# Performance work log

Hardware: AMD Instinct MI355X
Metric: run time of the kernel (lower is better)

The kernel has to match this reference:

```python
import jax, jax.numpy as jnp
import numpy as np

B, S, E = 64, 512, 1024   # batch, seq_len, enc_size (bert-large hidden)
P, K, C = 200, 10, 3      # num_prototypes, proto_size, num_classes


def setup_inputs() -> dict:
    key = jax.random.key(0)
    k1, k2, k3 = jax.random.split(key, 3)
    embedding = jax.random.normal(k1, (B, S, E), dtype=jnp.float32)
    # protolayer initialized with nn.init.uniform_ -> U[0,1)
    protolayer = jax.random.uniform(k2, (P, K, E), dtype=jnp.float32)
    fc_weight = jax.random.normal(k3, (C, P), dtype=jnp.float32) * 0.05
    return {"embedding": embedding, "protolayer": protolayer, "fc_weight": fc_weight}


def reference(embedding, protolayer, fc_weight):
    # torch.cdist(embedding[:,None], protolayer, p=2) broadcasts to [B,P,S,K]:
    # distances[b,p,s,k] = ||embedding[b,s,:] - protolayer[p,k,:]||_2
    x2 = jnp.sum(embedding * embedding, axis=-1)            # [B,S]
    y2 = jnp.sum(protolayer * protolayer, axis=-1)          # [P,K]
    xy = jnp.einsum('bse,pke->bpsk', embedding, protolayer) # [B,P,S,K]
    d2 = x2[:, None, :, None] + y2[None, :, None, :] - 2.0 * xy
    distances = jnp.sqrt(jnp.maximum(d2, 0.0))              # [B,P,S,K]
    # -max_pool2d(-d, kernel=(S,1)) == min over seq dim
    min_distances = jnp.min(distances, axis=2)               # [B,P,K]
    prototype_distances = jnp.mean(min_distances, axis=-1)   # [B,P]
    class_out = prototype_distances @ fc_weight.T            # [B,C]
    return prototype_distances, distances, class_out
```

## Files before the change

kernel.cpp:

```cpp
#include <hip/hip_runtime.h>
#include <hip/hip_bf16.h>

#define B_ 64
#define S_ 512
#define E_ 1024
#define P_ 200
#define K_ 10
#define C_ 3

#define BM 256
#define BN 80
#define BKS 64
#define NSTAGE (E_ / BKS)
#define NROWS_A (B_ * S_)
#define NROWS_B (P_ * K_)
#define NROWS_T (NROWS_A + NROWS_B)
#define NMT 128
#define NNT 25

typedef __attribute__((ext_vector_type(8))) short short8;
typedef __attribute__((ext_vector_type(4))) float f32x4;

__device__ __forceinline__ float bf2f(unsigned short u) {
    unsigned int x = ((unsigned int)u) << 16;
    return __uint_as_float(x);
}
__device__ __forceinline__ unsigned short f2bf(float f) {
    __hip_bfloat16 h = __float2bfloat16(f);
    unsigned short u;
    __builtin_memcpy(&u, &h, 2);
    return u;
}

__device__ __forceinline__ int swz(int row, int kbyte) {
    return (row * (BKS * 2) + kbyte) ^ ((row & 7) << 4);
}

#define GLDS16(gsrc, ldst)                                                              \
    __builtin_amdgcn_global_load_lds((const __attribute__((address_space(1))) unsigned int*)(gsrc), \
                                     (__attribute__((address_space(3))) unsigned int*)(ldst), 16, 0, 0)

__global__ __launch_bounds__(256) void preconvert(const float* __restrict__ emb,
                                                  const float* __restrict__ proto,
                                                  unsigned short* __restrict__ bf,
                                                  float* __restrict__ xy2) {
    const int row  = blockIdx.x * 4 + (threadIdx.x >> 6);
    const int lane = threadIdx.x & 63;
    const float* src = (row < NROWS_A) ? emb + (size_t)row * E_
                                       : proto + (size_t)(row - NROWS_A) * E_;
    unsigned short* dst = bf + (size_t)row * E_;
    float s = 0.f;
#pragma unroll
    for (int p = 0; p < 4; ++p) {
        float4 v = *(const float4*)(src + p * 256 + lane * 4);
        ushort4 h = { f2bf(v.x), f2bf(v.y), f2bf(v.z), f2bf(v.w) };
        float a = bf2f(h.x), b = bf2f(h.y), c = bf2f(h.z), d = bf2f(h.w);
        s += a * a + b * b + c * c + d * d;
        *(ushort4*)(dst + p * 256 + lane * 4) = h;
    }
#pragma unroll
    for (int off = 32; off > 0; off >>= 1) s += __shfl_xor(s, off);
    if (lane == 0) xy2[row] = s;
}

__global__ __launch_bounds__(512) void dist_gemm_bf(const unsigned short* __restrict__ Abf,
                                                    const unsigned short* __restrict__ Bbf,
                                                    const float* __restrict__ x2g,
                                                    const float* __restrict__ y2g,
                                                    float* __restrict__ dist,
                                                    float* __restrict__ ws_min) {
    __shared__ __align__(16) unsigned char smem[86016];
    __shared__ float red[8][BN];

    unsigned short* AsBase = (unsigned short*)smem;
    unsigned short* BsBase = (unsigned short*)(smem + 2 * BM * BKS * 2);
    float* Ch = (float*)smem;

    const int tid  = threadIdx.x;
    const int lane = tid & 63;
    const int wv   = tid >> 6;
    const int l15  = lane & 15;
    const int lh   = lane >> 4;

    const int id = blockIdx.x;
    const int sw = (id & 7) * (3200 / 8) + (id >> 3);
    const int nt = sw % NNT;
    const int mt = sw / NNT;

    const unsigned short* aSrc[4];
    unsigned lOffA[4];
#pragma unroll
    for (int i = 0; i < 4; ++i) {
        int idx = i * 512 + wv * 64 + lane;
        int r = idx >> 3, c = idx & 7;
        aSrc[i]  = Abf + (size_t)(mt * BM + r) * E_ + (c ^ (r & 7)) * 8;
        lOffA[i] = (unsigned)(i * 512 + wv * 64) * 8;
    }
    const unsigned short* bSrc[2];
    unsigned lOffB[2];
    {
        int idx = wv * 64 + lane;
        int r = idx >> 3, c = idx & 7;
        bSrc[0]  = Bbf + (size_t)(nt * BN + r) * E_ + (c ^ (r & 7)) * 8;
        lOffB[0] = (unsigned)(wv * 64) * 8;
    }
    {
        int idx = 512 + wv * 64 + lane;
        int r = idx >> 3, c = idx & 7;
        bSrc[1]  = Bbf + (size_t)(nt * BN + (r < BN ? r : 0)) * E_ + (c ^ (r & 7)) * 8;
        lOffB[1] = (unsigned)(512 + wv * 64) * 8;
    }

    f32x4 acc[2][5];
#pragma unroll
    for (int i = 0; i < 2; ++i)
#pragma unroll
        for (int j = 0; j < 5; ++j) acc[i][j] = (f32x4){0.f, 0.f, 0.f, 0.f};

#define ISSUE(tt, bb)                                                          \
    do {                                                                       \
        const size_t ko_ = (size_t)(tt) * BKS;                                 \
        unsigned short* Asb_ = AsBase + (bb) * (BM * BKS);                     \
        unsigned short* Bsb_ = BsBase + (bb) * (BN * BKS);                     \
        _Pragma("unroll")                                                      \
        for (int i_ = 0; i_ < 4; ++i_) GLDS16(aSrc[i_] + ko_, Asb_ + lOffA[i_]); \
        GLDS16(bSrc[0] + ko_, Bsb_ + lOffB[0]);                                \
        if (wv < 2) GLDS16(bSrc[1] + ko_, Bsb_ + lOffB[1]);                    \
    } while (0)

#define COMPUTE(bb)                                                            \
    do {                                                                       \
        const char* Ab_ = (const char*)(AsBase + (bb) * (BM * BKS));           \
        const char* Bb_ = (const char*)(BsBase + (bb) * (BN * BKS));           \
        _Pragma("unroll")                                                      \
        for (int kk = 0; kk < 2; ++kk) {                                       \
            const int kbyte = kk * 64 + lh * 16;                               \
            short8 af[2];                                                      \
            _Pragma("unroll")                                                  \
            for (int mf = 0; mf < 2; ++mf)                                     \
                af[mf] = *(const short8*)(Ab_ + swz(wv * 32 + mf * 16 + l15, kbyte)); \
            short8 bfr[5];                                                     \
            _Pragma("unroll")                                                  \
            for (int nf = 0; nf < 5; ++nf)                                     \
                bfr[nf] = *(const short8*)(Bb_ + swz(nf * 16 + l15, kbyte));   \
            _Pragma("unroll")                                                  \
            for (int mf = 0; mf < 2; ++mf)                                     \
                _Pragma("unroll")                                              \
                for (int nf = 0; nf < 5; ++nf)                                 \
                    acc[mf][nf] = __builtin_amdgcn_mfma_f32_16x16x32_bf16(     \
                        af[mf], bfr[nf], acc[mf][nf], 0, 0, 0);                \
        }                                                                      \
    } while (0)

    ISSUE(0, 0);
    __syncthreads();

    int buf = 0;
    for (int t = 0; t < NSTAGE; ++t) {
        if (t + 1 < NSTAGE) ISSUE(t + 1, buf ^ 1);
        COMPUTE(buf);
        __syncthreads();
        buf ^= 1;
    }
#undef ISSUE
#undef COMPUTE

    const int b  = mt >> 1;
    const int s0 = (mt & 1) * 256;

    float y2v[5];
#pragma unroll
    for (int nf = 0; nf < 5; ++nf) y2v[nf] = y2g[nt * BN + nf * 16 + l15];

    float mloc[5];
#pragma unroll
    for (int nf = 0; nf < 5; ++nf) mloc[nf] = 3.4e38f;

#define CH(blk, row, col) Ch[(((blk) * 16) + (row)) * 82 + (col)]

#pragma unroll
    for (int h = 0; h < 2; ++h) {
#pragma unroll
        for (int rg = 0; rg < 4; ++rg) {
            float x2 = x2g[mt * BM + wv * 32 + h * 16 + lh * 4 + rg];
#pragma unroll
            for (int nf = 0; nf < 5; ++nf) {
                float d2 = x2 + y2v[nf] - 2.f * acc[h][nf][rg];
                float d  = sqrtf(fmaxf(d2, 0.f));
                mloc[nf] = fminf(mloc[nf], d);
                CH(wv, lh * 4 + rg, nf * 16 + l15) = d;
            }
        }
        __syncthreads();

#pragma unroll
        for (int i = 0; i < 5; ++i) {
            int fid = i * 512 + tid;
            int r   = fid / 40;
            int q   = fid - r * 40;
            int p8  = r >> 3;
            int blk = r & 7;
            int e   = 4 * q;
            f32x4 v;
            v.x = CH(blk, (e + 0) / 10, p8 * 10 + (e + 0) % 10);
            v.y = CH(blk, (e + 1) / 10, p8 * 10 + (e + 1) % 10);
            v.z = CH(blk, (e + 2) / 10, p8 * 10 + (e + 2) % 10);
            v.w = CH(blk, (e + 3) / 10, p8 * 10 + (e + 3) % 10);
            int s_start = s0 + blk * 32 + h * 16;
            size_t base = ((size_t)(b * P_ + nt * 8 + p8) * S_ + s_start) * 10 + e;
            __builtin_nontemporal_store(v, (f32x4*)(dist + base));
        }
        __syncthreads();
    }
#undef CH

#pragma unroll
    for (int nf = 0; nf < 5; ++nf) {
        mloc[nf] = fminf(mloc[nf], __shfl_xor(mloc[nf], 16));
        mloc[nf] = fminf(mloc[nf], __shfl_xor(mloc[nf], 32));
    }
    if (lane < 16) {
#pragma unroll
        for (int nf = 0; nf < 5; ++nf) red[wv][nf * 16 + lane] = mloc[nf];
    }
    __syncthreads();
    if (tid < BN) {
        float v = red[0][tid];
#pragma unroll
        for (int w = 1; w < 8; ++w) v = fminf(v, red[w][tid]);
        ws_min[(size_t)mt * NROWS_B + nt * BN + tid] = v;
    }
}

__global__ __launch_bounds__(256) void mean_fc(const float* __restrict__ ws_min,
                                               const float* __restrict__ fcw,
                                               float* __restrict__ pd,
                                               float* __restrict__ cls) {
    const int b = blockIdx.x;
    const int t = threadIdx.x;
    __shared__ float pds[P_];
    if (t < P_) {
        float sum = 0.f;
#pragma unroll
        for (int k = 0; k < K_; ++k) {
            float m = fminf(ws_min[(size_t)(b * 2 + 0) * NROWS_B + t * K_ + k],
                            ws_min[(size_t)(b * 2 + 1) * NROWS_B + t * K_ + k]);
            sum += m;
        }
        float v = sum * (1.0f / K_);
        pd[b * P_ + t] = v;
        pds[t] = v;
    }
    __syncthreads();
    if (t < C_) {
        float s = 0.f;
        for (int p = 0; p < P_; ++p) s += pds[p] * fcw[t * P_ + p];
        cls[b * C_ + t] = s;
    }
}

#define FBM 128
#define FBN 80
#define FBKS 64
#define FNST 16
__device__ __forceinline__ int swzf(int row, int kbyte) {
    return (row * (FBKS * 2) + kbyte) ^ ((row & 7) << 4);
}
__global__ __launch_bounds__(256) void dist_mfma_fb(const float* __restrict__ emb,
                                                    const float* __restrict__ proto,
                                                    float* __restrict__ dist) {
    __shared__ short As[FBM * FBKS];
    __shared__ short Bs[FBN * FBKS];
    __shared__ float x2s[FBM];
    __shared__ float y2s[FBN];

    const int tid  = threadIdx.x;
    const int lane = tid & 63;
    const int wv   = tid >> 6;
    const int l15  = lane & 15;
    const int lh   = lane >> 4;

    const int id = blockIdx.x;
    const int sw = (id & 7) * (6400 / 8) + (id >> 3);
    const int nt = sw % 25;
    const int mt = sw / 25;

    const float* Ab = emb + (size_t)mt * FBM * E_ + (size_t)(tid >> 4) * E_ + (tid & 15) * 4;
    const float* Bb = proto + (size_t)nt * FBN * E_ + (size_t)(tid >> 4) * E_ + (tid & 15) * 4;

    f32x4 acc[2][5];
#pragma unroll
    for (int i = 0; i < 2; ++i)
#pragma unroll
        for (int j = 0; j < 5; ++j) acc[i][j] = (f32x4){0.f, 0.f, 0.f, 0.f};

    float x2p[8], y2p[5];
#pragma unroll
    for (int i = 0; i < 8; ++i) x2p[i] = 0.f;
#pragma unroll
    for (int i = 0; i < 5; ++i) y2p[i] = 0.f;

    float4 pa[8], pb[5];
#pragma unroll
    for (int i = 0; i < 8; ++i) pa[i] = *(const float4*)(Ab + (size_t)i * 16 * E_);
#pragma unroll
    for (int i = 0; i < 5; ++i) pb[i] = *(const float4*)(Bb + (size_t)i * 16 * E_);

    for (int t = 0; t < FNST; ++t) {
        ushort4 ca[8];
#pragma unroll
        for (int i = 0; i < 8; ++i) {
            float4 v = pa[i];
            x2p[i] += v.x * v.x + v.y * v.y + v.z * v.z + v.w * v.w;
            ca[i] = (ushort4){ f2bf(v.x), f2bf(v.y), f2bf(v.z), f2bf(v.w) };
        }
        ushort4 cb[5];
#pragma unroll
        for (int i = 0; i < 5; ++i) {
            float4 v = pb[i];
            y2p[i] += v.x * v.x + v.y * v.y + v.z * v.z + v.w * v.w;
            cb[i] = (ushort4){ f2bf(v.x), f2bf(v.y), f2bf(v.z), f2bf(v.w) };
        }
        __syncthreads();
#pragma unroll
        for (int i = 0; i < 8; ++i) {
            int idx = i * 256 + tid;
            *(ushort4*)((char*)As + swzf(idx >> 4, (idx & 15) * 8)) = ca[i];
        }
#pragma unroll
        for (int i = 0; i < 5; ++i) {
            int idx = i * 256 + tid;
            *(ushort4*)((char*)Bs + swzf(idx >> 4, (idx & 15) * 8)) = cb[i];
        }
        __syncthreads();
        if (t + 1 < FNST) {
            const float* An = Ab + (size_t)(t + 1) * FBKS;
            const float* Bn = Bb + (size_t)(t + 1) * FBKS;
#pragma unroll
            for (int i = 0; i < 8; ++i) pa[i] = *(const float4*)(An + (size_t)i * 16 * E_);
#pragma unroll
            for (int i = 0; i < 5; ++i) pb[i] = *(const float4*)(Bn + (size_t)i * 16 * E_);
        }
#pragma unroll
        for (int kk = 0; kk < 2; ++kk) {
            const int kbyte = kk * 64 + lh * 16;
            short8 af[2];
#pragma unroll
            for (int mf = 0; mf < 2; ++mf)
                af[mf] = *(const short8*)((const char*)As + swzf(wv * 32 + mf * 16 + l15, kbyte));
            short8 bfr[5];
#pragma unroll
            for (int nf = 0; nf < 5; ++nf)
                bfr[nf] = *(const short8*)((const char*)Bs + swzf(nf * 16 + l15, kbyte));
#pragma unroll
            for (int mf = 0; mf < 2; ++mf)
#pragma unroll
                for (int nf = 0; nf < 5; ++nf)
                    acc[mf][nf] = __builtin_amdgcn_mfma_f32_16x16x32_bf16(
                        af[mf], bfr[nf], acc[mf][nf], 0, 0, 0);
        }
    }

#pragma unroll
    for (int i = 0; i < 8; ++i) {
        float v = x2p[i];
        v += __shfl_xor(v, 1); v += __shfl_xor(v, 2);
        v += __shfl_xor(v, 4); v += __shfl_xor(v, 8);
        if (l15 == 0) x2s[16 * i + (tid >> 4)] = v;
    }
#pragma unroll
    for (int i = 0; i < 5; ++i) {
        float v = y2p[i];
        v += __shfl_xor(v, 1); v += __shfl_xor(v, 2);
        v += __shfl_xor(v, 4); v += __shfl_xor(v, 8);
        if (l15 == 0) y2s[16 * i + (tid >> 4)] = v;
    }
    __syncthreads();

#pragma unroll
    for (int mf = 0; mf < 2; ++mf) {
#pragma unroll
        for (int nf = 0; nf < 5; ++nf) {
#pragma unroll
            for (int rg = 0; rg < 4; ++rg) {
                int ml = wv * 32 + mf * 16 + lh * 4 + rg;
                int nl = nf * 16 + l15;
                int m = mt * FBM + ml;
                int n = nt * FBN + nl;
                int b = m >> 9;
                int s = m & (S_ - 1);
                int p = n / K_;
                int k = n - p * K_;
                float d2 = x2s[ml] + y2s[nl] - 2.f * acc[mf][nf][rg];
                dist[(((size_t)b * P_ + p) * S_ + s) * K_ + k] = sqrtf(fmaxf(d2, 0.f));
            }
        }
    }
}

__global__ __launch_bounds__(256) void min_mean(const float* __restrict__ dist,
                                                float* __restrict__ pd) {
    const int p = blockIdx.x;
    const int b = blockIdx.y;
    const float* dp = dist + ((size_t)b * P_ + p) * (size_t)(S_ * K_);
    const int tid = threadIdx.x;

    const float4* base = (const float4*)(dp + (size_t)tid * 20);
    float4 q0 = base[0], q1 = base[1], q2 = base[2], q3 = base[3], q4 = base[4];

    float mn[K_];
    mn[0] = fminf(q0.x, q2.z); mn[1] = fminf(q0.y, q2.w);
    mn[2] = fminf(q0.z, q3.x); mn[3] = fminf(q0.w, q3.y);
    mn[4] = fminf(q1.x, q3.z); mn[5] = fminf(q1.y, q3.w);
    mn[6] = fminf(q1.z, q4.x); mn[7] = fminf(q1.w, q4.y);
    mn[8] = fminf(q2.x, q4.z); mn[9] = fminf(q2.y, q4.w);

#pragma unroll
    for (int k = 0; k < K_; ++k) {
#pragma unroll
        for (int off = 32; off > 0; off >>= 1)
            mn[k] = fminf(mn[k], __shfl_xor(mn[k], off));
    }

    __shared__ float red[4][K_];
    if ((tid & 63) == 0) {
#pragma unroll
        for (int k = 0; k < K_; ++k) red[tid >> 6][k] = mn[k];
    }
    __syncthreads();
    if (tid == 0) {
        float sum = 0.f;
#pragma unroll
        for (int k = 0; k < K_; ++k)
            sum += fminf(fminf(red[0][k], red[1][k]), fminf(red[2][k], red[3][k]));
        pd[b * P_ + p] = sum * (1.0f / K_);
    }
}

__global__ void fc_kernel(const float* __restrict__ pd, const float* __restrict__ fc,
                          float* __restrict__ cls) {
    int tid = threadIdx.x;
    if (tid < B_ * C_) {
        int b = tid / C_;
        int c = tid % C_;
        float s = 0.f;
        for (int p = 0; p < P_; ++p) s += pd[b * P_ + p] * fc[c * P_ + p];
        cls[b * C_ + c] = s;
    }
}

extern "C" void kernel_launch(void* const* d_in, const int* in_sizes, int n_in,
                              void* d_out, int out_size, void* d_ws, size_t ws_size,
                              hipStream_t stream) {
    const float* emb   = (const float*)d_in[0];
    const float* proto = (const float*)d_in[1];
    const float* fc    = (const float*)d_in[2];
    float* out = (float*)d_out;

    float* pd   = out;
    float* dist = out + (size_t)B_ * P_;
    float* cls  = out + (size_t)B_ * P_ + (size_t)B_ * P_ * S_ * K_;

    const size_t bf_bytes  = (size_t)NROWS_T * E_ * 2;
    const size_t xy2_bytes = (size_t)NROWS_T * 4;
    const size_t min_bytes = (size_t)NMT * NROWS_B * 4;
    const size_t ws_need   = bf_bytes + xy2_bytes + min_bytes;

    if (ws_size >= ws_need) {
        unsigned short* bf = (unsigned short*)d_ws;
        float* xy2    = (float*)((char*)d_ws + bf_bytes);
        float* ws_min = (float*)((char*)d_ws + bf_bytes + xy2_bytes);
        preconvert<<<NROWS_T / 4, 256, 0, stream>>>(emb, proto, bf, xy2);
        dist_gemm_bf<<<NMT * NNT, 512, 0, stream>>>(bf, bf + (size_t)NROWS_A * E_,
                                                    xy2, xy2 + NROWS_A, dist, ws_min);
        mean_fc<<<B_, 256, 0, stream>>>(ws_min, fc, pd, cls);
    } else {
        dist_mfma_fb<<<6400, 256, 0, stream>>>(emb, proto, dist);
        min_mean<<<dim3(P_, B_), 256, 0, stream>>>(dist, pd);
        fc_kernel<<<1, 256, 0, stream>>>(pd, fc, cls);
    }
}
```

Baseline: 292.6 us.

## Double GEMM N-tile to 160 with 4x2 wave layout and zero-padded prototypes

Widens the distance GEMM tile from 80 to 160 prototype rows. Waves are rearranged into a 4x2 grid, each computing a 64x80 sub-tile, so every A tile loaded into LDS is reused across twice as many columns and A-side global and LDS traffic is halved. Prototype rows are zero-padded up to 13*160 in the preconvert kernel, and the epilogue skips stores for padded prototypes. In exchange the kernel needs more LDS and accumulator registers, launches fewer blocks, and spends some work on padding.

```diff
diff --git a/kernel.cpp b/kernel.cpp
--- a/kernel.cpp
+++ b/kernel.cpp
@@ -9,14 +9,15 @@
 #define C_ 3
 
 #define BM 256
-#define BN 80
+#define BN 160
 #define BKS 64
 #define NSTAGE (E_ / BKS)
 #define NROWS_A (B_ * S_)
 #define NROWS_B (P_ * K_)
-#define NROWS_T (NROWS_A + NROWS_B)
 #define NMT 128
-#define NNT 25
+#define NNT 13
+#define NBPAD (NNT * BN)
+#define NROWS_P (NROWS_A + NBPAD)
 
 typedef __attribute__((ext_vector_type(8))) short short8;
 typedef __attribute__((ext_vector_type(4))) float f32x4;
@@ -46,9 +47,17 @@
                                                   float* __restrict__ xy2) {
     const int row  = blockIdx.x * 4 + (threadIdx.x >> 6);
     const int lane = threadIdx.x & 63;
+    unsigned short* dst = bf + (size_t)row * E_;
+
+    if (row >= NROWS_A + NROWS_B) {
+        ushort4 z = {0, 0, 0, 0};
+#pragma unroll
+        for (int p = 0; p < 4; ++p) *(ushort4*)(dst + p * 256 + lane * 4) = z;
+        if (lane == 0) xy2[row] = 0.f;
+        return;
+    }
     const float* src = (row < NROWS_A) ? emb + (size_t)row * E_
                                        : proto + (size_t)(row - NROWS_A) * E_;
-    unsigned short* dst = bf + (size_t)row * E_;
     float s = 0.f;
 #pragma unroll
     for (int p = 0; p < 4; ++p) {
@@ -69,8 +78,8 @@
                                                     const float* __restrict__ y2g,
                                                     float* __restrict__ dist,
                                                     float* __restrict__ ws_min) {
-    __shared__ __align__(16) unsigned char smem[86016];
-    __shared__ float red[8][BN];
+    __shared__ __align__(16) unsigned char smem[106496];
+    __shared__ float red[8][80];
 
     unsigned short* AsBase = (unsigned short*)smem;
     unsigned short* BsBase = (unsigned short*)(smem + 2 * BM * BKS * 2);
@@ -79,11 +88,13 @@
     const int tid  = threadIdx.x;
     const int lane = tid & 63;
     const int wv   = tid >> 6;
+    const int wm   = wv >> 1;
+    const int wn   = wv & 1;
     const int l15  = lane & 15;
     const int lh   = lane >> 4;
 
     const int id = blockIdx.x;
-    const int sw = (id & 7) * (3200 / 8) + (id >> 3);
+    const int sw = (id & 7) * (1664 / 8) + (id >> 3);
     const int nt = sw % NNT;
     const int mt = sw / NNT;
 
@@ -91,29 +102,30 @@
     unsigned lOffA[4];
 #pragma unroll
     for (int i = 0; i < 4; ++i) {
-        int idx = i * 512 + wv * 64 + lane;
+        int idx = i * 512 + tid;
         int r = idx >> 3, c = idx & 7;
         aSrc[i]  = Abf + (size_t)(mt * BM + r) * E_ + (c ^ (r & 7)) * 8;
         lOffA[i] = (unsigned)(i * 512 + wv * 64) * 8;
     }
-    const unsigned short* bSrc[2];
-    unsigned lOffB[2];
+    const unsigned short* bSrc[3];
+    unsigned lOffB[3];
+#pragma unroll
+    for (int i = 0; i < 2; ++i) {
+        int idx = i * 512 + tid;
+        int r = idx >> 3, c = idx & 7;
+        bSrc[i]  = Bbf + (size_t)(nt * BN + r) * E_ + (c ^ (r & 7)) * 8;
+        lOffB[i] = (unsigned)(i * 512 + wv * 64) * 8;
+    }
     {
-        int idx = wv * 64 + lane;
+        int idx = 1024 + wv * 64 + lane;
         int r = idx >> 3, c = idx & 7;
-        bSrc[0]  = Bbf + (size_t)(nt * BN + r) * E_ + (c ^ (r & 7)) * 8;
-        lOffB[0] = (unsigned)(wv * 64) * 8;
-    }
-    {
-        int idx = 512 + wv * 64 + lane;
-        int r = idx >> 3, c = idx & 7;
-        bSrc[1]  = Bbf + (size_t)(nt * BN + (r < BN ? r : 0)) * E_ + (c ^ (r & 7)) * 8;
-        lOffB[1] = (unsigned)(512 + wv * 64) * 8;
-    }
-
-    f32x4 acc[2][5];
-#pragma unroll
-    for (int i = 0; i < 2; ++i)
+        bSrc[2]  = Bbf + (size_t)(nt * BN + (r < BN ? r : 0)) * E_ + (c ^ (r & 7)) * 8;
+        lOffB[2] = (unsigned)(1024 + wv * 64) * 8;
+    }
+
+    f32x4 acc[4][5];
+#pragma unroll
+    for (int i = 0; i < 4; ++i)
 #pragma unroll
         for (int j = 0; j < 5; ++j) acc[i][j] = (f32x4){0.f, 0.f, 0.f, 0.f};
 
@@ -124,8 +136,9 @@
         unsigned short* Bsb_ = BsBase + (bb) * (BN * BKS);                     \
         _Pragma("unroll")                                                      \
         for (int i_ = 0; i_ < 4; ++i_) GLDS16(aSrc[i_] + ko_, Asb_ + lOffA[i_]); \
-        GLDS16(bSrc[0] + ko_, Bsb_ + lOffB[0]);                                \
-        if (wv < 2) GLDS16(bSrc[1] + ko_, Bsb_ + lOffB[1]);                    \
+        _Pragma("unroll")                                                      \
+        for (int i_ = 0; i_ < 2; ++i_) GLDS16(bSrc[i_] + ko_, Bsb_ + lOffB[i_]); \
+        if (wv < 4) GLDS16(bSrc[2] + ko_, Bsb_ + lOffB[2]);                    \
     } while (0)
 
 #define COMPUTE(bb)                                                            \
@@ -135,16 +148,16 @@
         _Pragma("unroll")                                                      \
         for (int kk = 0; kk < 2; ++kk) {                                       \
             const int kbyte = kk * 64 + lh * 16;                               \
-            short8 af[2];                                                      \
+            short8 af[4];                                                      \
             _Pragma("unroll")                                                  \
-            for (int mf = 0; mf < 2; ++mf)                                     \
-                af[mf] = *(const short8*)(Ab_ + swz(wv * 32 + mf * 16 + l15, kbyte)); \
+            for (int mf = 0; mf < 4; ++mf)                                     \
+                af[mf] = *(const short8*)(Ab_ + swz(wm * 64 + mf * 16 + l15, kbyte)); \
             short8 bfr[5];                                                     \
             _Pragma("unroll")                                                  \
             for (int nf = 0; nf < 5; ++nf)                                     \
-                bfr[nf] = *(const short8*)(Bb_ + swz(nf * 16 + l15, kbyte));   \
+                bfr[nf] = *(const short8*)(Bb_ + swz(wn * 80 + nf * 16 + l15, kbyte)); \
             _Pragma("unroll")                                                  \
-            for (int mf = 0; mf < 2; ++mf)                                     \
+            for (int mf = 0; mf < 4; ++mf)                                     \
                 _Pragma("unroll")                                              \
                 for (int nf = 0; nf < 5; ++nf)                                 \
                     acc[mf][nf] = __builtin_amdgcn_mfma_f32_16x16x32_bf16(     \
@@ -170,25 +183,25 @@
 
     float y2v[5];
 #pragma unroll
-    for (int nf = 0; nf < 5; ++nf) y2v[nf] = y2g[nt * BN + nf * 16 + l15];
+    for (int nf = 0; nf < 5; ++nf) y2v[nf] = y2g[nt * BN + wn * 80 + nf * 16 + l15];
 
     float mloc[5];
 #pragma unroll
     for (int nf = 0; nf < 5; ++nf) mloc[nf] = 3.4e38f;
 
-#define CH(blk, row, col) Ch[(((blk) * 16) + (row)) * 82 + (col)]
-
-#pragma unroll
-    for (int h = 0; h < 2; ++h) {
+#define CH(slab, row, col) Ch[(((slab) * 16) + (row)) * 162 + (col)]
+
+#pragma unroll
+    for (int mf = 0; mf < 4; ++mf) {
 #pragma unroll
         for (int rg = 0; rg < 4; ++rg) {
-            float x2 = x2g[mt * BM + wv * 32 + h * 16 + lh * 4 + rg];
+            float x2 = x2g[mt * BM + wm * 64 + mf * 16 + lh * 4 + rg];
 #pragma unroll
             for (int nf = 0; nf < 5; ++nf) {
-                float d2 = x2 + y2v[nf] - 2.f * acc[h][nf][rg];
+                float d2 = x2 + y2v[nf] - 2.f * acc[mf][nf][rg];
                 float d  = sqrtf(fmaxf(d2, 0.f));
                 mloc[nf] = fminf(mloc[nf], d);
-                CH(wv, lh * 4 + rg, nf * 16 + l15) = d;
+                CH(wm, lh * 4 + rg, wn * 80 + nf * 16 + l15) = d;
             }
         }
         __syncthreads();
@@ -198,17 +211,20 @@
             int fid = i * 512 + tid;
             int r   = fid / 40;
             int q   = fid - r * 40;
-            int p8  = r >> 3;
-            int blk = r & 7;
+            int p16 = r >> 2;
+            int slab= r & 3;
             int e   = 4 * q;
-            f32x4 v;
-            v.x = CH(blk, (e + 0) / 10, p8 * 10 + (e + 0) % 10);
-            v.y = CH(blk, (e + 1) / 10, p8 * 10 + (e + 1) % 10);
-            v.z = CH(blk, (e + 2) / 10, p8 * 10 + (e + 2) % 10);
-            v.w = CH(blk, (e + 3) / 10, p8 * 10 + (e + 3) % 10);
-            int s_start = s0 + blk * 32 + h * 16;
-            size_t base = ((size_t)(b * P_ + nt * 8 + p8) * S_ + s_start) * 10 + e;
-            __builtin_nontemporal_store(v, (f32x4*)(dist + base));
+            int p   = nt * 16 + p16;
+            if (p < P_) {
+                f32x4 v;
+                v.x = CH(slab, (e + 0) / 10, p16 * 10 + (e + 0) % 10);
+                v.y = CH(slab, (e + 1) / 10, p16 * 10 + (e + 1) % 10);
+                v.z = CH(slab, (e + 2) / 10, p16 * 10 + (e + 2) % 10);
+                v.w = CH(slab, (e + 3) / 10, p16 * 10 + (e + 3) % 10);
+                int s_start = s0 + slab * 64 + mf * 16;
+                size_t base = ((size_t)(b * P_ + p) * S_ + s_start) * 10 + e;
+                __builtin_nontemporal_store(v, (f32x4*)(dist + base));
+            }
         }
         __syncthreads();
     }
@@ -225,10 +241,11 @@
     }
     __syncthreads();
     if (tid < BN) {
-        float v = red[0][tid];
-#pragma unroll
-        for (int w = 1; w < 8; ++w) v = fminf(v, red[w][tid]);
-        ws_min[(size_t)mt * NROWS_B + nt * BN + tid] = v;
+        int wn_ = tid / 80;
+        int cl  = tid - wn_ * 80;
+        float v = fminf(fminf(red[0 * 2 + wn_][cl], red[1 * 2 + wn_][cl]),
+                        fminf(red[2 * 2 + wn_][cl], red[3 * 2 + wn_][cl]));
+        ws_min[(size_t)mt * NBPAD + nt * BN + tid] = v;
     }
 }
 
@@ -243,8 +260,8 @@
         float sum = 0.f;
 #pragma unroll
         for (int k = 0; k < K_; ++k) {
-            float m = fminf(ws_min[(size_t)(b * 2 + 0) * NROWS_B + t * K_ + k],
-                            ws_min[(size_t)(b * 2 + 1) * NROWS_B + t * K_ + k]);
+            float m = fminf(ws_min[(size_t)(b * 2 + 0) * NBPAD + t * K_ + k],
+                            ws_min[(size_t)(b * 2 + 1) * NBPAD + t * K_ + k]);
             sum += m;
         }
         float v = sum * (1.0f / K_);
@@ -461,16 +478,16 @@
     float* dist = out + (size_t)B_ * P_;
     float* cls  = out + (size_t)B_ * P_ + (size_t)B_ * P_ * S_ * K_;
 
-    const size_t bf_bytes  = (size_t)NROWS_T * E_ * 2;
-    const size_t xy2_bytes = (size_t)NROWS_T * 4;
-    const size_t min_bytes = (size_t)NMT * NROWS_B * 4;
+    const size_t bf_bytes  = (size_t)NROWS_P * E_ * 2;
+    const size_t xy2_bytes = (size_t)NROWS_P * 4;
+    const size_t min_bytes = (size_t)NMT * NBPAD * 4;
     const size_t ws_need   = bf_bytes + xy2_bytes + min_bytes;
 
     if (ws_size >= ws_need) {
         unsigned short* bf = (unsigned short*)d_ws;
         float* xy2    = (float*)((char*)d_ws + bf_bytes);
         float* ws_min = (float*)((char*)d_ws + bf_bytes + xy2_bytes);
-        preconvert<<<NROWS_T / 4, 256, 0, stream>>>(emb, proto, bf, xy2);
+        preconvert<<<NROWS_P / 4, 256, 0, stream>>>(emb, proto, bf, xy2);
         dist_gemm_bf<<<NMT * NNT, 512, 0, stream>>>(bf, bf + (size_t)NROWS_A * E_,
                                                     xy2, xy2 + NROWS_A, dist, ws_min);
         mean_fc<<<B_, 256, 0, stream>>>(ws_min, fc, pd, cls);
```

Measured after the change: 236.0 us (median of 3 runs). -19.4%, faster.
